# Kernel tuning notes

Hardware: AMD Instinct MI355X
Metric: run time of the kernel (lower is better)

Reference implementation:

```python
import jax, jax.numpy as jnp
import numpy as np

B, N, C = 16, 1024, 768
D = 512
DEPTH = 4
K = 3
HP = WP = 32
A_EPS = 1e-4
POW_MIN = 1e-20
LN_EPS = 1e-5


def setup_inputs() -> dict:
    key = jax.random.key(0)
    ks = jax.random.split(key, 20)
    inp = {
        "tokens": jax.random.normal(ks[0], (B, N, C), dtype=jnp.float32),
        "in_proj_w": jax.random.normal(ks[1], (C, D), dtype=jnp.float32) * 0.02,
        "in_proj_b": jnp.zeros((D,), dtype=jnp.float32),
        "blk_norm_w": jnp.ones((DEPTH, D), dtype=jnp.float32),
        "blk_norm_b": jnp.zeros((DEPTH, D), dtype=jnp.float32),
        "blk_inp_w": jax.random.normal(ks[2], (DEPTH, D, 2 * D), dtype=jnp.float32) * 0.02,
        "blk_inp_b": jnp.zeros((DEPTH, 2 * D), dtype=jnp.float32),
        "blk_conv_w": jax.random.normal(ks[3], (DEPTH, K, K, 1, D), dtype=jnp.float32) * 0.1,
        "blk_conv_b": jnp.zeros((DEPTH, D), dtype=jnp.float32),
        "blk_a_logit": jax.random.normal(ks[4], (DEPTH, D), dtype=jnp.float32) * 0.1,
        "blk_b": jnp.ones((DEPTH, D), dtype=jnp.float32) + jax.random.normal(ks[5], (DEPTH, D), dtype=jnp.float32) * 0.02,
        "blk_c": jnp.ones((DEPTH, D), dtype=jnp.float32) + jax.random.normal(ks[6], (DEPTH, D), dtype=jnp.float32) * 0.02,
        "blk_d": jnp.ones((DEPTH, D), dtype=jnp.float32) + jax.random.normal(ks[7], (DEPTH, D), dtype=jnp.float32) * 0.02,
        "blk_out_w": jax.random.normal(ks[8], (DEPTH, D, D), dtype=jnp.float32) * 0.02,
        "blk_out_b": jnp.zeros((DEPTH, D), dtype=jnp.float32),
        "out_norm_w": jnp.ones((D,), dtype=jnp.float32),
        "out_norm_b": jnp.zeros((D,), dtype=jnp.float32),
    }
    return inp


def _layernorm(x, w, b):
    mu = jnp.mean(x, axis=-1, keepdims=True)
    var = jnp.var(x, axis=-1, keepdims=True)
    return (x - mu) * jax.lax.rsqrt(var + LN_EPS) * w + b


def _ssm_scan(x, a_logit, bb, cc, dd):
    # x: (B', L, D)   s_t = a s_{t-1} + b x_t ; y_t = c s_t + d x_t  (log-domain cumsum form)
    L = x.shape[1]
    a = jnp.clip(jax.nn.sigmoid(a_logit), A_EPS, 1.0 - A_EPS)
    t = jnp.arange(L, dtype=jnp.float32)
    a_pow = jnp.maximum(jnp.exp(t[:, None] * jnp.log(a)[None, :]), POW_MIN)  # (L, D)
    u = x * bb  # (B', L, D)
    r = jnp.cumsum(u / a_pow[None], axis=1)
    s = r * a_pow[None]
    return s * cc + x * dd


def _scan2d(x, a_logit, bb, cc, dd):
    # x: (B, H, W, D); bidirectional row-major + col-major scans, averaged
    Bb, H, W, Dd = x.shape
    L = H * W
    seq_row = x.reshape(Bb, L, Dd)
    seq_col = jnp.transpose(x, (0, 2, 1, 3)).reshape(Bb, L, Dd)
    seqs = jnp.concatenate([seq_row, seq_col], axis=0)            # (2B, L, D)
    all_seqs = jnp.concatenate([seqs, seqs[:, ::-1]], axis=0)     # (4B, L, D)
    y2 = _ssm_scan(all_seqs, a_logit, bb, cc, dd)
    y_f, y_rev = jnp.split(y2, 2, axis=0)
    y = 0.5 * (y_f + y_rev[:, ::-1])
    y_row, y_col = jnp.split(y, 2, axis=0)
    y_row_map = y_row.reshape(Bb, H, W, Dd)
    y_col_map = jnp.transpose(y_col.reshape(Bb, W, H, Dd), (0, 2, 1, 3))
    return 0.5 * (y_row_map + y_col_map)


def _dwconv_silu(x, kernel, bias):
    # x: (B,H,W,D); kernel: (K,K,1,D) depthwise; SAME padding (odd k)
    y = jax.lax.conv_general_dilated(
        x, kernel, window_strides=(1, 1), padding="SAME",
        feature_group_count=x.shape[-1],
        dimension_numbers=("NHWC", "HWIO", "NHWC"))
    return jax.nn.silu(y + bias)


def _block(x, nw, nb, iw, ib, cw, cb, al, sb, sc, sd, ow, ob):
    h = _layernorm(x, nw, nb)
    xg = h @ iw + ib                      # (B,H,W,2D)
    x_in, gate = jnp.split(xg, 2, axis=-1)
    gate = jax.nn.sigmoid(gate)
    u = _dwconv_silu(x_in, cw, cb)
    y = _scan2d(u, al, sb, sc, sd)
    y = (y * gate) @ ow + ob
    return x + y


def reference(tokens, in_proj_w, in_proj_b, blk_norm_w, blk_norm_b, blk_inp_w,
              blk_inp_b, blk_conv_w, blk_conv_b, blk_a_logit, blk_b, blk_c,
              blk_d, blk_out_w, blk_out_b, out_norm_w, out_norm_b):
    x = tokens @ in_proj_w + in_proj_b          # (B, N, D)
    x = x.reshape(B, HP, WP, D)                 # token grid
    for i in range(DEPTH):
        x = _block(x, blk_norm_w[i], blk_norm_b[i], blk_inp_w[i], blk_inp_b[i],
                   blk_conv_w[i], blk_conv_b[i], blk_a_logit[i], blk_b[i],
                   blk_c[i], blk_d[i], blk_out_w[i], blk_out_b[i])
    x = _layernorm(x, out_norm_w, out_norm_b)
    return jnp.mean(x, axis=(1, 2))             # pooled global vector (B, D)
```

## Files before the change

kernel.cpp:

```cpp
#include <hip/hip_runtime.h>
#include <hip/hip_bf16.h>
#include <math.h>

#define NPOS 16384
#define DD   512
#define PP   ((size_t)NPOS * DD)

typedef __bf16 bf16x8 __attribute__((ext_vector_type(8)));
typedef float  f32x4  __attribute__((ext_vector_type(4)));

__device__ __forceinline__ void gload16(const __bf16* g, __bf16* l) {
  __builtin_amdgcn_global_load_lds((__attribute__((address_space(1))) void*)(g),
                                   (__attribute__((address_space(3))) void*)(l), 16, 0, 0);
}
__device__ __forceinline__ void wait_vm0() { asm volatile("s_waitcnt vmcnt(0)" ::: "memory"); }
__device__ __forceinline__ void wait_vm4() { asm volatile("s_waitcnt vmcnt(4)" ::: "memory"); }
__device__ __forceinline__ void wait_lgkm0() { asm volatile("s_waitcnt lgkmcnt(0)" ::: "memory"); }

__global__ __launch_bounds__(256, 3) void gemm_k(
    const __bf16* __restrict__ A, const __bf16* __restrict__ Bt,
    const float* __restrict__ bias, const float* __restrict__ res,
    float* __restrict__ C0, __bf16* __restrict__ C1, __bf16* __restrict__ C1b,
    int N, int K, int epi)
{
  __shared__ __bf16 Asm[3][128 * 32];
  __shared__ __bf16 Bsm[3][128 * 32];

  const int tid  = threadIdx.x;
  const int w    = tid >> 6;
  const int lane = tid & 63;
  const int quad = lane >> 4;
  const int l16  = lane & 15;
  const int wm   = (w >> 1) << 6;
  const int wn   = (w & 1) << 6;

  const int nwg = gridDim.x;
  const int cpx = nwg >> 3;
  const int lin = (blockIdx.x & 7) * cpx + (blockIdx.x >> 3);
  const int nbn = N >> 7;
  const int sh  = (nbn == 8) ? 3 : 2;
  const int mt  = lin >> sh;
  const int ntc = lin & (nbn - 1);
  const int bm  = mt << 7;
  const int bn  = ntc << 7;

  const __bf16* Ab = A  + (size_t)bm * K;
  const __bf16* Bb = Bt + (size_t)bn * K;
  const int nk = K >> 5;

  f32x4 acc[4][4];
  #pragma unroll
  for (int i = 0; i < 4; ++i)
    #pragma unroll
    for (int j = 0; j < 4; ++j) acc[i][j] = (f32x4){0.f, 0.f, 0.f, 0.f};

  #define STG(P, gb, tile, buf, k2) {                                           \
    const int ch_ = tid + ((k2) << 8);                                          \
    const int r_ = ch_ >> 2, c_ = ch_ & 3;                                      \
    gload16(gb + (size_t)r_ * K + ((tile) << 5) + ((c_ ^ ((r_ >> 1) & 3)) << 3),\
            &P[buf][ch_ << 3]);                                                 \
  }

  STG(Asm, Ab, 0, 0, 0) STG(Asm, Ab, 0, 0, 1)
  STG(Bsm, Bb, 0, 0, 0) STG(Bsm, Bb, 0, 0, 1)
  STG(Asm, Ab, 1, 1, 0) STG(Asm, Ab, 1, 1, 1)
  STG(Bsm, Bb, 1, 1, 0) STG(Bsm, Bb, 1, 1, 1)
  wait_vm4();
  __builtin_amdgcn_s_barrier();

  int cur = 0;
  for (int t = 0; t < nk; ++t) {
    const int nx2 = (cur == 0) ? 2 : cur - 1;
    const bool st = (t + 2 < nk);

    if (st) {
      STG(Asm, Ab, t + 2, nx2, 0) STG(Asm, Ab, t + 2, nx2, 1)
      STG(Bsm, Bb, t + 2, nx2, 0) STG(Bsm, Bb, t + 2, nx2, 1)
    }

    bf16x8 af[4], bfr[4];
    #pragma unroll
    for (int i = 0; i < 4; ++i) {
      const int m = wm + i * 16 + l16;
      af[i] = *(const bf16x8*)(&Asm[cur][m * 32 + ((quad ^ ((m >> 1) & 3)) << 3)]);
    }
    #pragma unroll
    for (int j = 0; j < 4; ++j) {
      const int n = wn + j * 16 + l16;
      bfr[j] = *(const bf16x8*)(&Bsm[cur][n * 32 + ((quad ^ ((n >> 1) & 3)) << 3)]);
    }

    __builtin_amdgcn_s_setprio(1);
    #pragma unroll
    for (int i = 0; i < 4; ++i)
      #pragma unroll
      for (int j = 0; j < 4; ++j)
        acc[i][j] = __builtin_amdgcn_mfma_f32_16x16x32_bf16(af[i], bfr[j], acc[i][j], 0, 0, 0);
    __builtin_amdgcn_s_setprio(0);

    if (st) { wait_vm4(); } else { wait_vm0(); }
    __builtin_amdgcn_s_barrier();
    cur = (cur == 2) ? 0 : cur + 1;
  }
  #undef STG

  if (epi == 1) {
    const bool dosig = (bn >= 512);
    __bf16* dst = dosig ? C1 : C1b;
    const int cb = dosig ? (bn - 512) : bn;
    char* wb = (char*)Asm + w * 9216;
    #pragma unroll
    for (int i = 0; i < 4; ++i)
      #pragma unroll
      for (int j = 0; j < 4; ++j) {
        const float bv = bias[bn + wn + j * 16 + l16];
        #pragma unroll
        for (int r = 0; r < 4; ++r) {
          float v = acc[i][j][r] + bv;
          if (dosig) v = 1.f / (1.f + expf(-v));
          *(__bf16*)(wb + (i * 16 + quad * 4 + r) * 144 + (j * 16 + l16) * 2) = (__bf16)v;
        }
      }
    wait_lgkm0();
    #pragma unroll
    for (int i = 0; i < 4; ++i)
      #pragma unroll
      for (int h = 0; h < 2; ++h) {
        const int rr = (lane >> 3) + h * 8;
        bf16x8 vv = *(bf16x8*)(wb + (i * 16 + rr) * 144 + (lane & 7) * 16);
        const int grow = bm + wm + i * 16 + rr;
        *(bf16x8*)(dst + (size_t)grow * 512 + cb + wn + (lane & 7) * 8) = vv;
      }
  } else {
    #pragma unroll
    for (int j = 0; j < 4; ++j) {
      const int col = wn + j * 16 + l16;
      const float bv = bias[bn + col];
      #pragma unroll
      for (int i = 0; i < 4; ++i) {
        const int row0 = bm + wm + i * 16 + quad * 4;
        #pragma unroll
        for (int r = 0; r < 4; ++r) {
          float v = acc[i][j][r] + bv;
          size_t off = (size_t)(row0 + r) * N + bn + col;
          if (epi == 2) v += res[off];
          C0[off] = v;
        }
      }
    }
  }
}

__global__ __launch_bounds__(256) void cvt_k(const float* __restrict__ s, __bf16* __restrict__ d)
{
  size_t i = ((size_t)blockIdx.x * 256 + threadIdx.x) * 8;
  float4 a = *(const float4*)(s + i);
  float4 b = *(const float4*)(s + i + 4);
  bf16x8 v;
  v[0] = (__bf16)a.x; v[1] = (__bf16)a.y; v[2] = (__bf16)a.z; v[3] = (__bf16)a.w;
  v[4] = (__bf16)b.x; v[5] = (__bf16)b.y; v[6] = (__bf16)b.z; v[7] = (__bf16)b.w;
  *(bf16x8*)(d + i) = v;
}

__global__ __launch_bounds__(256) void tr_k(const float* __restrict__ src, __bf16* __restrict__ dst,
                                            int K, int N, size_t sstr, size_t dstr)
{
  __shared__ float t[32][33];
  const float* s = src + blockIdx.z * sstr;
  __bf16* d = dst + blockIdx.z * dstr;
  int n0 = blockIdx.x * 32, k0 = blockIdx.y * 32;
  int tx = threadIdx.x & 31, ty = threadIdx.x >> 5;
  #pragma unroll
  for (int i = 0; i < 4; ++i)
    t[ty + i * 8][tx] = s[(size_t)(k0 + ty + i * 8) * N + n0 + tx];
  __syncthreads();
  #pragma unroll
  for (int i = 0; i < 4; ++i)
    d[(size_t)(n0 + ty + i * 8) * K + k0 + tx] = (__bf16)t[tx][ty + i * 8];
}

__global__ __launch_bounds__(256) void ln_k(const float* __restrict__ x, const float* __restrict__ w,
                                            const float* __restrict__ bv, __bf16* __restrict__ out)
{
  int gw = (blockIdx.x * 256 + threadIdx.x) >> 6;
  int lane = threadIdx.x & 63;
  const float* xp = x + ((size_t)gw << 9) + lane * 8;
  float4 u0 = *(const float4*)xp;
  float4 u1 = *(const float4*)(xp + 4);
  float v[8] = {u0.x,u0.y,u0.z,u0.w,u1.x,u1.y,u1.z,u1.w};
  float s = 0.f;
  #pragma unroll
  for (int j = 0; j < 8; ++j) s += v[j];
  #pragma unroll
  for (int off = 32; off; off >>= 1) s += __shfl_xor(s, off, 64);
  float mu = s * (1.f/512.f);
  float q = 0.f;
  #pragma unroll
  for (int j = 0; j < 8; ++j) { float d = v[j] - mu; q += d*d; }
  #pragma unroll
  for (int off = 32; off; off >>= 1) q += __shfl_xor(q, off, 64);
  float rstd = rsqrtf(q * (1.f/512.f) + 1e-5f);
  int dch = lane * 8;
  float4 w0 = *(const float4*)(w + dch),  w1 = *(const float4*)(w + dch + 4);
  float4 b0 = *(const float4*)(bv + dch), b1 = *(const float4*)(bv + dch + 4);
  float wv[8] = {w0.x,w0.y,w0.z,w0.w,w1.x,w1.y,w1.z,w1.w};
  float bb[8] = {b0.x,b0.y,b0.z,b0.w,b1.x,b1.y,b1.z,b1.w};
  bf16x8 ov;
  #pragma unroll
  for (int j = 0; j < 8; ++j) ov[j] = (__bf16)((v[j] - mu) * rstd * wv[j] + bb[j]);
  *(bf16x8*)(out + ((size_t)gw << 9) + dch) = ov;
}

__device__ __forceinline__ float sig_a(float al) {
  float a = 1.f / (1.f + expf(-al));
  return fminf(fmaxf(a, 1e-4f), 1.f - 1e-4f);
}

__global__ __launch_bounds__(512, 2) void scan2d_k(
    const __bf16* __restrict__ xin, const float* __restrict__ cw, const float* __restrict__ cb,
    const float* __restrict__ alog, const float* __restrict__ bvec, const float* __restrict__ cvec,
    const float* __restrict__ dvec, const __bf16* __restrict__ gate, __bf16* __restrict__ yo)
{
  __shared__ __bf16 T[32768];
  __shared__ __bf16 Y[32768];
  __shared__ float  S[4][32][32];
  const int tid = threadIdx.x;
  const int cg  = blockIdx.x;
  const int b   = blockIdx.y;
  const int ch  = tid & 31;
  const int c0  = tid >> 5;
  const int c1  = c0 + 16;
  const int d   = (cg << 5) + ch;

  const float a   = sig_a(alog[d]);
  const float lna = logf(a);
  const float ia  = 1.f / a;
  const float bb  = bvec[d];
  const float sc  = 0.25f * cvec[d];
  const float dd  = dvec[d];

  const __bf16* ub = xin + ((size_t)b << 19) + (cg << 5);

  #pragma unroll
  for (int i = 0; i < 8; ++i) {
    int flat = (tid + i * 512) << 3;
    int pos = flat >> 5;
    int c8  = flat & 31;
    *(bf16x8*)(T + flat) = *(const bf16x8*)(ub + (size_t)pos * 512 + c8);
  }
  float w00 = cw[(0 << 9) + d], w01 = cw[(1 << 9) + d], w02 = cw[(2 << 9) + d];
  float w10 = cw[(3 << 9) + d], w11 = cw[(4 << 9) + d], w12 = cw[(5 << 9) + d];
  float w20 = cw[(6 << 9) + d], w21 = cw[(7 << 9) + d], w22 = cw[(8 << 9) + d];
  const float cbv = cb[d];
  const float A0f = expf((float)(c0 << 5) * lna),        R0f = expf((float)(c0 << 5) * -lna);
  const float A1f = expf((float)(c1 << 5) * lna),        R1f = expf((float)(c1 << 5) * -lna);
  const float A0b = expf((float)((31 - c0) << 5) * lna), R0b = expf((float)((31 - c0) << 5) * -lna);
  const float A1b = expf((float)((31 - c1) << 5) * lna), R1b = expf((float)((31 - c1) << 5) * -lna);
  __syncthreads();

  {
    const bool up0 = (c0 > 0);
    const bool dn1 = (c0 < 15);
    float a0 = 0.f, a1 = 0.f, a2 = 0.f, f0 = 0.f, f1 = 0.f, f2 = 0.f;
    float b0 = up0 ? (float)T[(((c0 - 1) << 5)) * 32 + ch] : 0.f;
    float b1 =        (float)T[((c0 << 5)) * 32 + ch];
    float b2 =        (float)T[(((c0 + 1) << 5)) * 32 + ch];
    float g0 =        (float)T[(((c1 - 1) << 5)) * 32 + ch];
    float g1 =        (float)T[((c1 << 5)) * 32 + ch];
    float g2 = dn1 ? (float)T[(((c1 + 1) << 5)) * 32 + ch] : 0.f;
    #pragma unroll 4
    for (int ww = 0; ww < 32; ++ww) {
      float e0 = 0.f, e1 = 0.f, e2 = 0.f, i0 = 0.f, i1 = 0.f, i2 = 0.f;
      if (ww < 31) {
        e0 = up0 ? (float)T[(((c0 - 1) << 5) + ww + 1) * 32 + ch] : 0.f;
        e1 =        (float)T[((c0 << 5) + ww + 1) * 32 + ch];
        e2 =        (float)T[(((c0 + 1) << 5) + ww + 1) * 32 + ch];
        i0 =        (float)T[(((c1 - 1) << 5) + ww + 1) * 32 + ch];
        i1 =        (float)T[((c1 << 5) + ww + 1) * 32 + ch];
        i2 = dn1 ? (float)T[(((c1 + 1) << 5) + ww + 1) * 32 + ch] : 0.f;
      }
      float acc0 = cbv, acc1 = cbv;
      acc0 = fmaf(a0, w00, acc0); acc0 = fmaf(b0, w01, acc0); acc0 = fmaf(e0, w02, acc0);
      acc0 = fmaf(a1, w10, acc0); acc0 = fmaf(b1, w11, acc0); acc0 = fmaf(e1, w12, acc0);
      acc0 = fmaf(a2, w20, acc0); acc0 = fmaf(b2, w21, acc0); acc0 = fmaf(e2, w22, acc0);
      acc1 = fmaf(f0, w00, acc1); acc1 = fmaf(g0, w01, acc1); acc1 = fmaf(i0, w02, acc1);
      acc1 = fmaf(f1, w10, acc1); acc1 = fmaf(g1, w11, acc1); acc1 = fmaf(i1, w12, acc1);
      acc1 = fmaf(f2, w20, acc1); acc1 = fmaf(g2, w21, acc1); acc1 = fmaf(i2, w22, acc1);
      acc0 = acc0 / (1.f + expf(-acc0));
      acc1 = acc1 / (1.f + expf(-acc1));
      Y[((c0 << 5) + ww) * 32 + ch] = (__bf16)acc0;
      Y[((c1 << 5) + ww) * 32 + ch] = (__bf16)acc1;
      a0 = b0; a1 = b1; a2 = b2; b0 = e0; b1 = e1; b2 = e2;
      f0 = g0; f1 = g1; f2 = g2; g0 = i0; g1 = i1; g2 = i2;
    }
  }
  __syncthreads();

  #define STEP(r_, uu_, apr_, rp_)                                 \
    { float rr_ = (apr_ < 1e-20f) ? 1e20f : rp_;                   \
      r_ = fmaf((uu_) * bb, rr_, r_); }

  {
    float p0 = A0f, q0 = R0f, p0B = A0b, q0B = R0b;
    float p1 = A1f, q1 = R1f, p1B = A1b, q1B = R1b;
    float s0 = 0.f, s1 = 0.f, s2 = 0.f, s3 = 0.f;
    float s4 = 0.f, s5 = 0.f, s6 = 0.f, s7 = 0.f;
    #pragma unroll 4
    for (int j = 0; j < 32; ++j) {
      float u0rf = (float)Y[((c0 << 5) + j) * 32 + ch];
      float u0rb = (float)Y[((c0 << 5) + (31 - j)) * 32 + ch];
      float u0cf = (float)Y[((j << 5) | c0) * 32 + ch];
      float u0cb = (float)Y[(((31 - j) << 5) | c0) * 32 + ch];
      float u1rf = (float)Y[((c1 << 5) + j) * 32 + ch];
      float u1rb = (float)Y[((c1 << 5) + (31 - j)) * 32 + ch];
      float u1cf = (float)Y[((j << 5) | c1) * 32 + ch];
      float u1cb = (float)Y[(((31 - j) << 5) | c1) * 32 + ch];
      STEP(s0, u0rf, p0, q0)  STEP(s2, u0cf, p0, q0)
      STEP(s1, u0rb, p0B, q0B) STEP(s3, u0cb, p0B, q0B)
      STEP(s4, u1rf, p1, q1)  STEP(s6, u1cf, p1, q1)
      STEP(s5, u1rb, p1B, q1B) STEP(s7, u1cb, p1B, q1B)
      p0 *= a; q0 *= ia; p0B *= a; q0B *= ia;
      p1 *= a; q1 *= ia; p1B *= a; q1B *= ia;
    }
    S[0][c0][ch] = s0; S[1][c0][ch] = s1; S[2][c0][ch] = s2; S[3][c0][ch] = s3;
    S[0][c1][ch] = s4; S[1][c1][ch] = s5; S[2][c1][ch] = s6; S[3][c1][ch] = s7;
  }
  __syncthreads();

  if (tid < 128) {
    int arr = tid >> 5, ch2 = tid & 31;
    float run = 0.f;
    if ((arr & 1) == 0) {
      #pragma unroll 4
      for (int cc = 0; cc < 32; ++cc) { float v = S[arr][cc][ch2]; S[arr][cc][ch2] = run; run += v; }
    } else {
      #pragma unroll 4
      for (int cc = 31; cc >= 0; --cc) { float v = S[arr][cc][ch2]; S[arr][cc][ch2] = run; run += v; }
    }
  }
  __syncthreads();

  {
    float r0 = S[2][c0][ch], r1 = S[2][c1][ch];
    float p0 = A0f, q0 = R0f, p1 = A1f, q1 = R1f;
    #pragma unroll 4
    for (int j = 0; j < 32; ++j) {
      int i0 = ((j << 5) | c0) * 32 + ch, i1 = ((j << 5) | c1) * 32 + ch;
      float u0 = (float)Y[i0], u1 = (float)Y[i1];
      float ap0 = fmaxf(p0, 1e-20f), ap1 = fmaxf(p1, 1e-20f);
      STEP(r0, u0, p0, q0) STEP(r1, u1, p1, q1)
      T[i0] = (__bf16)(r0 * ap0);
      T[i1] = (__bf16)(r1 * ap1);
      p0 *= a; q0 *= ia; p1 *= a; q1 *= ia;
    }
  }
  {
    float r0 = S[3][c0][ch], r1 = S[3][c1][ch];
    float p0 = A0b, q0 = R0b, p1 = A1b, q1 = R1b;
    #pragma unroll 4
    for (int j = 31; j >= 0; --j) {
      int i0 = ((j << 5) | c0) * 32 + ch, i1 = ((j << 5) | c1) * 32 + ch;
      float u0 = (float)Y[i0], u1 = (float)Y[i1];
      float ap0 = fmaxf(p0, 1e-20f), ap1 = fmaxf(p1, 1e-20f);
      STEP(r0, u0, p0, q0) STEP(r1, u1, p1, q1)
      T[i0] = (__bf16)(sc * ((float)T[i0] + r0 * ap0));
      T[i1] = (__bf16)(sc * ((float)T[i1] + r1 * ap1));
      p0 *= a; q0 *= ia; p1 *= a; q1 *= ia;
    }
  }
  __syncthreads();

  {
    float r0 = S[0][c0][ch], r1 = S[0][c1][ch];
    float p0 = A0f, q0 = R0f, p1 = A1f, q1 = R1f;
    #pragma unroll 4
    for (int j = 0; j < 32; ++j) {
      int i0 = ((c0 << 5) + j) * 32 + ch, i1 = ((c1 << 5) + j) * 32 + ch;
      float u0 = (float)Y[i0], u1 = (float)Y[i1];
      float ap0 = fmaxf(p0, 1e-20f), ap1 = fmaxf(p1, 1e-20f);
      STEP(r0, u0, p0, q0) STEP(r1, u1, p1, q1)
      T[i0] = (__bf16)((float)T[i0] + sc * (r0 * ap0));
      T[i1] = (__bf16)((float)T[i1] + sc * (r1 * ap1));
      p0 *= a; q0 *= ia; p1 *= a; q1 *= ia;
    }
  }
  {
    const __bf16* gb = gate + ((size_t)b << 19) + (cg << 5) + ch;
    __bf16* yb = yo + ((size_t)b << 19) + (cg << 5) + ch;
    float r0 = S[1][c0][ch], r1 = S[1][c1][ch];
    float p0 = A0b, q0 = R0b, p1 = A1b, q1 = R1b;
    #pragma unroll 4
    for (int j = 31; j >= 0; --j) {
      int pp0 = (c0 << 5) + j, pp1 = (c1 << 5) + j;
      int i0 = pp0 * 32 + ch, i1 = pp1 * 32 + ch;
      float u0 = (float)Y[i0], u1 = (float)Y[i1];
      float ap0 = fmaxf(p0, 1e-20f), ap1 = fmaxf(p1, 1e-20f);
      STEP(r0, u0, p0, q0) STEP(r1, u1, p1, q1)
      float y0 = (float)T[i0] + sc * (r0 * ap0) + dd * u0;
      float y1 = (float)T[i1] + sc * (r1 * ap1) + dd * u1;
      yb[(size_t)pp0 * 512] = (__bf16)(y0 * (float)gb[(size_t)pp0 * 512]);
      yb[(size_t)pp1 * 512] = (__bf16)(y1 * (float)gb[(size_t)pp1 * 512]);
      p0 *= a; q0 *= ia; p1 *= a; q1 *= ia;
    }
  }
  #undef STEP
}

__global__ __launch_bounds__(256) void reduce_k(const __bf16* __restrict__ hn, float* __restrict__ out)
{
  __shared__ float part[4][64];
  int l = threadIdx.x & 63;
  int q = threadIdx.x >> 6;
  int d = blockIdx.y * 64 + l;
  int b = blockIdx.x;
  const __bf16* p = hn + ((size_t)b << 19) + d + ((size_t)(q * 256) << 9);
  float s0 = 0.f, s1 = 0.f, s2 = 0.f, s3 = 0.f;
  for (int t = 0; t < 256; t += 4) {
    s0 += (float)p[(size_t)(t+0) << 9];
    s1 += (float)p[(size_t)(t+1) << 9];
    s2 += (float)p[(size_t)(t+2) << 9];
    s3 += (float)p[(size_t)(t+3) << 9];
  }
  part[q][l] = (s0 + s1) + (s2 + s3);
  __syncthreads();
  if (threadIdx.x < 64)
    out[b * 512 + d] = (part[0][l] + part[1][l] + part[2][l] + part[3][l]) * (1.f / 1024.f);
}

extern "C" void kernel_launch(void* const* d_in, const int* in_sizes, int n_in,
                              void* d_out, int out_size, void* d_ws, size_t ws_size,
                              hipStream_t stream)
{
  const float* tokens = (const float*)d_in[0];
  const float* in_w   = (const float*)d_in[1];
  const float* in_b   = (const float*)d_in[2];
  const float* nw     = (const float*)d_in[3];
  const float* nb     = (const float*)d_in[4];
  const float* iw     = (const float*)d_in[5];
  const float* ib     = (const float*)d_in[6];
  const float* cw     = (const float*)d_in[7];
  const float* cb     = (const float*)d_in[8];
  const float* al     = (const float*)d_in[9];
  const float* bbv    = (const float*)d_in[10];
  const float* ccv    = (const float*)d_in[11];
  const float* ddv    = (const float*)d_in[12];
  const float* ow     = (const float*)d_in[13];
  const float* obv    = (const float*)d_in[14];
  const float* onw    = (const float*)d_in[15];
  const float* onb    = (const float*)d_in[16];

  float*  x     = (float*)d_ws;
  __bf16* hy16  = (__bf16*)(x + PP);
  __bf16* xin16 = hy16 + PP;
  __bf16* g16   = xin16 + PP;
  __bf16* iwT   = g16 + PP;
  __bf16* owT   = iwT + (size_t)4 * 1024 * 512;
  __bf16* tb16  = owT + (size_t)4 * 512 * 512;
  __bf16* inwT  = xin16;

  cvt_k<<<6144, 256, 0, stream>>>(tokens, tb16);
  tr_k<<<dim3(16, 24, 1), 256, 0, stream>>>(in_w, inwT, 768, 512, 0, 0);
  tr_k<<<dim3(32, 16, 4), 256, 0, stream>>>(iw, iwT, 512, 1024, (size_t)512*1024, (size_t)1024*512);
  tr_k<<<dim3(16, 16, 4), 256, 0, stream>>>(ow, owT, 512, 512, (size_t)512*512, (size_t)512*512);

  gemm_k<<<512, 256, 0, stream>>>(tb16, inwT, in_b, nullptr, x, nullptr, nullptr,
                                  512, 768, 0);

  for (int i = 0; i < 4; ++i) {
    ln_k<<<4096, 256, 0, stream>>>(x, nw + i*512, nb + i*512, hy16);
    gemm_k<<<1024, 256, 0, stream>>>(hy16, iwT + (size_t)i*1024*512, ib + i*1024,
                                     nullptr, nullptr, g16, xin16, 1024, 512, 1);
    scan2d_k<<<dim3(16, 16), 512, 0, stream>>>(xin16, cw + i*9*512, cb + i*512,
                                               al + i*512, bbv + i*512, ccv + i*512,
                                               ddv + i*512, g16, hy16);
    gemm_k<<<512, 256, 0, stream>>>(hy16, owT + (size_t)i*512*512, obv + i*512,
                                    x, x, nullptr, nullptr, 512, 512, 2);
  }

  ln_k<<<4096, 256, 0, stream>>>(x, onw, onb, hy16);
  reduce_k<<<dim3(16, 8), 256, 0, stream>>>(hy16, (float*)d_out);
}
```

Before: 641.1 us.

## Split scan2d into 16-channel blocks with padded LDS rows and more occupancy

The 2D scan kernel now processes 16 channels per block instead of 32, launching twice as many blocks (32x16). Each thread owns one grid row/column instead of two, which halves per-thread work and register pressure, and launch bounds move to 4 blocks per CU. Shared-memory tiles are stored with a padded row stride (544) to reduce bank conflicts, and block-to-channel-group mapping is permuted. The trade-offs are less per-thread ILP, narrower 16-byte global loads per position, and smaller per-block coalescing width for the gated output writes.

```diff
diff --git a/kernel.cpp b/kernel.cpp
--- a/kernel.cpp
+++ b/kernel.cpp
@@ -216,21 +216,23 @@
   return fminf(fmaxf(a, 1e-4f), 1.f - 1e-4f);
 }
 
-__global__ __launch_bounds__(512, 2) void scan2d_k(
+#define CST 544
+
+__global__ __launch_bounds__(512, 4) void scan2d_k(
     const __bf16* __restrict__ xin, const float* __restrict__ cw, const float* __restrict__ cb,
     const float* __restrict__ alog, const float* __restrict__ bvec, const float* __restrict__ cvec,
     const float* __restrict__ dvec, const __bf16* __restrict__ gate, __bf16* __restrict__ yo)
 {
-  __shared__ __bf16 T[32768];
-  __shared__ __bf16 Y[32768];
-  __shared__ float  S[4][32][32];
+  __shared__ __bf16 T[32 * CST];
+  __shared__ __bf16 Y[32 * CST];
+  __shared__ float  S[4][32][16];
   const int tid = threadIdx.x;
-  const int cg  = blockIdx.x;
+  const int bx  = blockIdx.x;
+  const int cg  = ((bx & 7) << 2) | (bx >> 3);
   const int b   = blockIdx.y;
-  const int ch  = tid & 31;
-  const int c0  = tid >> 5;
-  const int c1  = c0 + 16;
-  const int d   = (cg << 5) + ch;
+  const int ch  = tid & 15;
+  const int c0  = tid >> 4;
+  const int d   = (cg << 4) + ch;
 
   const float a   = sig_a(alog[d]);
   const float lna = logf(a);
@@ -239,59 +241,45 @@
   const float sc  = 0.25f * cvec[d];
   const float dd  = dvec[d];
 
-  const __bf16* ub = xin + ((size_t)b << 19) + (cg << 5);
-
-  #pragma unroll
-  for (int i = 0; i < 8; ++i) {
-    int flat = (tid + i * 512) << 3;
-    int pos = flat >> 5;
-    int c8  = flat & 31;
-    *(bf16x8*)(T + flat) = *(const bf16x8*)(ub + (size_t)pos * 512 + c8);
+  const __bf16* ub = xin + ((size_t)b << 19) + (cg << 4);
+
+  #pragma unroll
+  for (int i = 0; i < 4; ++i) {
+    int f = tid + i * 512;
+    int pos = f >> 1, half = f & 1;
+    *(bf16x8*)(T + (pos >> 5) * CST + ((pos & 31) << 4) + (half << 3))
+        = *(const bf16x8*)(ub + (size_t)pos * 512 + (half << 3));
   }
   float w00 = cw[(0 << 9) + d], w01 = cw[(1 << 9) + d], w02 = cw[(2 << 9) + d];
   float w10 = cw[(3 << 9) + d], w11 = cw[(4 << 9) + d], w12 = cw[(5 << 9) + d];
   float w20 = cw[(6 << 9) + d], w21 = cw[(7 << 9) + d], w22 = cw[(8 << 9) + d];
   const float cbv = cb[d];
   const float A0f = expf((float)(c0 << 5) * lna),        R0f = expf((float)(c0 << 5) * -lna);
-  const float A1f = expf((float)(c1 << 5) * lna),        R1f = expf((float)(c1 << 5) * -lna);
   const float A0b = expf((float)((31 - c0) << 5) * lna), R0b = expf((float)((31 - c0) << 5) * -lna);
-  const float A1b = expf((float)((31 - c1) << 5) * lna), R1b = expf((float)((31 - c1) << 5) * -lna);
-  __syncthreads();
-
-  {
-    const bool up0 = (c0 > 0);
-    const bool dn1 = (c0 < 15);
-    float a0 = 0.f, a1 = 0.f, a2 = 0.f, f0 = 0.f, f1 = 0.f, f2 = 0.f;
-    float b0 = up0 ? (float)T[(((c0 - 1) << 5)) * 32 + ch] : 0.f;
-    float b1 =        (float)T[((c0 << 5)) * 32 + ch];
-    float b2 =        (float)T[(((c0 + 1) << 5)) * 32 + ch];
-    float g0 =        (float)T[(((c1 - 1) << 5)) * 32 + ch];
-    float g1 =        (float)T[((c1 << 5)) * 32 + ch];
-    float g2 = dn1 ? (float)T[(((c1 + 1) << 5)) * 32 + ch] : 0.f;
+  __syncthreads();
+
+  {
+    const bool up = (c0 > 0);
+    const bool dn = (c0 < 31);
+    float a0 = 0.f, a1 = 0.f, a2 = 0.f;
+    float b0 = up ? (float)T[(c0 - 1) * CST + ch] : 0.f;
+    float b1 =      (float)T[c0 * CST + ch];
+    float b2 = dn ? (float)T[(c0 + 1) * CST + ch] : 0.f;
     #pragma unroll 4
     for (int ww = 0; ww < 32; ++ww) {
-      float e0 = 0.f, e1 = 0.f, e2 = 0.f, i0 = 0.f, i1 = 0.f, i2 = 0.f;
+      float e0 = 0.f, e1 = 0.f, e2 = 0.f;
       if (ww < 31) {
-        e0 = up0 ? (float)T[(((c0 - 1) << 5) + ww + 1) * 32 + ch] : 0.f;
-        e1 =        (float)T[((c0 << 5) + ww + 1) * 32 + ch];
-        e2 =        (float)T[(((c0 + 1) << 5) + ww + 1) * 32 + ch];
-        i0 =        (float)T[(((c1 - 1) << 5) + ww + 1) * 32 + ch];
-        i1 =        (float)T[((c1 << 5) + ww + 1) * 32 + ch];
-        i2 = dn1 ? (float)T[(((c1 + 1) << 5) + ww + 1) * 32 + ch] : 0.f;
+        e0 = up ? (float)T[(c0 - 1) * CST + ((ww + 1) << 4) + ch] : 0.f;
+        e1 =      (float)T[c0 * CST + ((ww + 1) << 4) + ch];
+        e2 = dn ? (float)T[(c0 + 1) * CST + ((ww + 1) << 4) + ch] : 0.f;
       }
-      float acc0 = cbv, acc1 = cbv;
+      float acc0 = cbv;
       acc0 = fmaf(a0, w00, acc0); acc0 = fmaf(b0, w01, acc0); acc0 = fmaf(e0, w02, acc0);
       acc0 = fmaf(a1, w10, acc0); acc0 = fmaf(b1, w11, acc0); acc0 = fmaf(e1, w12, acc0);
       acc0 = fmaf(a2, w20, acc0); acc0 = fmaf(b2, w21, acc0); acc0 = fmaf(e2, w22, acc0);
-      acc1 = fmaf(f0, w00, acc1); acc1 = fmaf(g0, w01, acc1); acc1 = fmaf(i0, w02, acc1);
-      acc1 = fmaf(f1, w10, acc1); acc1 = fmaf(g1, w11, acc1); acc1 = fmaf(i1, w12, acc1);
-      acc1 = fmaf(f2, w20, acc1); acc1 = fmaf(g2, w21, acc1); acc1 = fmaf(i2, w22, acc1);
       acc0 = acc0 / (1.f + expf(-acc0));
-      acc1 = acc1 / (1.f + expf(-acc1));
-      Y[((c0 << 5) + ww) * 32 + ch] = (__bf16)acc0;
-      Y[((c1 << 5) + ww) * 32 + ch] = (__bf16)acc1;
+      Y[c0 * CST + (ww << 4) + ch] = (__bf16)acc0;
       a0 = b0; a1 = b1; a2 = b2; b0 = e0; b1 = e1; b2 = e2;
-      f0 = g0; f1 = g1; f2 = g2; g0 = i0; g1 = i1; g2 = i2;
     }
   }
   __syncthreads();
@@ -301,34 +289,24 @@
       r_ = fmaf((uu_) * bb, rr_, r_); }
 
   {
-    float p0 = A0f, q0 = R0f, p0B = A0b, q0B = R0b;
-    float p1 = A1f, q1 = R1f, p1B = A1b, q1B = R1b;
+    float pf = A0f, qf = R0f, pb = A0b, qb = R0b;
     float s0 = 0.f, s1 = 0.f, s2 = 0.f, s3 = 0.f;
-    float s4 = 0.f, s5 = 0.f, s6 = 0.f, s7 = 0.f;
     #pragma unroll 4
     for (int j = 0; j < 32; ++j) {
-      float u0rf = (float)Y[((c0 << 5) + j) * 32 + ch];
-      float u0rb = (float)Y[((c0 << 5) + (31 - j)) * 32 + ch];
-      float u0cf = (float)Y[((j << 5) | c0) * 32 + ch];
-      float u0cb = (float)Y[(((31 - j) << 5) | c0) * 32 + ch];
-      float u1rf = (float)Y[((c1 << 5) + j) * 32 + ch];
-      float u1rb = (float)Y[((c1 << 5) + (31 - j)) * 32 + ch];
-      float u1cf = (float)Y[((j << 5) | c1) * 32 + ch];
-      float u1cb = (float)Y[(((31 - j) << 5) | c1) * 32 + ch];
-      STEP(s0, u0rf, p0, q0)  STEP(s2, u0cf, p0, q0)
-      STEP(s1, u0rb, p0B, q0B) STEP(s3, u0cb, p0B, q0B)
-      STEP(s4, u1rf, p1, q1)  STEP(s6, u1cf, p1, q1)
-      STEP(s5, u1rb, p1B, q1B) STEP(s7, u1cb, p1B, q1B)
-      p0 *= a; q0 *= ia; p0B *= a; q0B *= ia;
-      p1 *= a; q1 *= ia; p1B *= a; q1B *= ia;
+      float urf = (float)Y[c0 * CST + (j << 4) + ch];
+      float urb = (float)Y[c0 * CST + ((31 - j) << 4) + ch];
+      float ucf = (float)Y[j * CST + (c0 << 4) + ch];
+      float ucb = (float)Y[(31 - j) * CST + (c0 << 4) + ch];
+      STEP(s0, urf, pf, qf)  STEP(s2, ucf, pf, qf)
+      STEP(s1, urb, pb, qb)  STEP(s3, ucb, pb, qb)
+      pf *= a; qf *= ia; pb *= a; qb *= ia;
     }
     S[0][c0][ch] = s0; S[1][c0][ch] = s1; S[2][c0][ch] = s2; S[3][c0][ch] = s3;
-    S[0][c1][ch] = s4; S[1][c1][ch] = s5; S[2][c1][ch] = s6; S[3][c1][ch] = s7;
-  }
-  __syncthreads();
-
-  if (tid < 128) {
-    int arr = tid >> 5, ch2 = tid & 31;
+  }
+  __syncthreads();
+
+  if (tid < 64) {
+    int arr = tid >> 4, ch2 = tid & 15;
     float run = 0.f;
     if ((arr & 1) == 0) {
       #pragma unroll 4
@@ -341,66 +319,61 @@
   __syncthreads();
 
   {
-    float r0 = S[2][c0][ch], r1 = S[2][c1][ch];
-    float p0 = A0f, q0 = R0f, p1 = A1f, q1 = R1f;
+    float r = S[2][c0][ch];
+    float p = A0f, q = R0f;
     #pragma unroll 4
     for (int j = 0; j < 32; ++j) {
-      int i0 = ((j << 5) | c0) * 32 + ch, i1 = ((j << 5) | c1) * 32 + ch;
-      float u0 = (float)Y[i0], u1 = (float)Y[i1];
-      float ap0 = fmaxf(p0, 1e-20f), ap1 = fmaxf(p1, 1e-20f);
-      STEP(r0, u0, p0, q0) STEP(r1, u1, p1, q1)
-      T[i0] = (__bf16)(r0 * ap0);
-      T[i1] = (__bf16)(r1 * ap1);
-      p0 *= a; q0 *= ia; p1 *= a; q1 *= ia;
-    }
-  }
-  {
-    float r0 = S[3][c0][ch], r1 = S[3][c1][ch];
-    float p0 = A0b, q0 = R0b, p1 = A1b, q1 = R1b;
+      int i0 = j * CST + (c0 << 4) + ch;
+      float u = (float)Y[i0];
+      float ap = fmaxf(p, 1e-20f);
+      STEP(r, u, p, q)
+      T[i0] = (__bf16)(r * ap);
+      p *= a; q *= ia;
+    }
+  }
+  {
+    float r = S[3][c0][ch];
+    float p = A0b, q = R0b;
     #pragma unroll 4
     for (int j = 31; j >= 0; --j) {
-      int i0 = ((j << 5) | c0) * 32 + ch, i1 = ((j << 5) | c1) * 32 + ch;
-      float u0 = (float)Y[i0], u1 = (float)Y[i1];
-      float ap0 = fmaxf(p0, 1e-20f), ap1 = fmaxf(p1, 1e-20f);
-      STEP(r0, u0, p0, q0) STEP(r1, u1, p1, q1)
-      T[i0] = (__bf16)(sc * ((float)T[i0] + r0 * ap0));
-      T[i1] = (__bf16)(sc * ((float)T[i1] + r1 * ap1));
-      p0 *= a; q0 *= ia; p1 *= a; q1 *= ia;
-    }
-  }
-  __syncthreads();
-
-  {
-    float r0 = S[0][c0][ch], r1 = S[0][c1][ch];
-    float p0 = A0f, q0 = R0f, p1 = A1f, q1 = R1f;
+      int i0 = j * CST + (c0 << 4) + ch;
+      float u = (float)Y[i0];
+      float ap = fmaxf(p, 1e-20f);
+      STEP(r, u, p, q)
+      T[i0] = (__bf16)(sc * ((float)T[i0] + r * ap));
+      p *= a; q *= ia;
+    }
+  }
+  __syncthreads();
+
+  {
+    float r = S[0][c0][ch];
+    float p = A0f, q = R0f;
     #pragma unroll 4
     for (int j = 0; j < 32; ++j) {
-      int i0 = ((c0 << 5) + j) * 32 + ch, i1 = ((c1 << 5) + j) * 32 + ch;
-      float u0 = (float)Y[i0], u1 = (float)Y[i1];
-      float ap0 = fmaxf(p0, 1e-20f), ap1 = fmaxf(p1, 1e-20f);
-      STEP(r0, u0, p0, q0) STEP(r1, u1, p1, q1)
-      T[i0] = (__bf16)((float)T[i0] + sc * (r0 * ap0));
-      T[i1] = (__bf16)((float)T[i1] + sc * (r1 * ap1));
-      p0 *= a; q0 *= ia; p1 *= a; q1 *= ia;
-    }
-  }
-  {
-    const __bf16* gb = gate + ((size_t)b << 19) + (cg << 5) + ch;
-    __bf16* yb = yo + ((size_t)b << 19) + (cg << 5) + ch;
-    float r0 = S[1][c0][ch], r1 = S[1][c1][ch];
-    float p0 = A0b, q0 = R0b, p1 = A1b, q1 = R1b;
+      int i0 = c0 * CST + (j << 4) + ch;
+      float u = (float)Y[i0];
+      float ap = fmaxf(p, 1e-20f);
+      STEP(r, u, p, q)
+      T[i0] = (__bf16)((float)T[i0] + sc * (r * ap));
+      p *= a; q *= ia;
+    }
+  }
+  {
+    const __bf16* gb = gate + ((size_t)b << 19) + (cg << 4) + ch;
+    __bf16* yb = yo + ((size_t)b << 19) + (cg << 4) + ch;
+    float r = S[1][c0][ch];
+    float p = A0b, q = R0b;
     #pragma unroll 4
     for (int j = 31; j >= 0; --j) {
-      int pp0 = (c0 << 5) + j, pp1 = (c1 << 5) + j;
-      int i0 = pp0 * 32 + ch, i1 = pp1 * 32 + ch;
-      float u0 = (float)Y[i0], u1 = (float)Y[i1];
-      float ap0 = fmaxf(p0, 1e-20f), ap1 = fmaxf(p1, 1e-20f);
-      STEP(r0, u0, p0, q0) STEP(r1, u1, p1, q1)
-      float y0 = (float)T[i0] + sc * (r0 * ap0) + dd * u0;
-      float y1 = (float)T[i1] + sc * (r1 * ap1) + dd * u1;
-      yb[(size_t)pp0 * 512] = (__bf16)(y0 * (float)gb[(size_t)pp0 * 512]);
-      yb[(size_t)pp1 * 512] = (__bf16)(y1 * (float)gb[(size_t)pp1 * 512]);
-      p0 *= a; q0 *= ia; p1 *= a; q1 *= ia;
+      int pp = (c0 << 5) + j;
+      int i0 = c0 * CST + (j << 4) + ch;
+      float u = (float)Y[i0];
+      float ap = fmaxf(p, 1e-20f);
+      STEP(r, u, p, q)
+      float y0 = (float)T[i0] + sc * (r * ap) + dd * u;
+      yb[(size_t)pp * 512] = (__bf16)(y0 * (float)gb[(size_t)pp * 512]);
+      p *= a; q *= ia;
     }
   }
   #undef STEP
@@ -470,7 +443,7 @@
     ln_k<<<4096, 256, 0, stream>>>(x, nw + i*512, nb + i*512, hy16);
     gemm_k<<<1024, 256, 0, stream>>>(hy16, iwT + (size_t)i*1024*512, ib + i*1024,
                                      nullptr, nullptr, g16, xin16, 1024, 512, 1);
-    scan2d_k<<<dim3(16, 16), 512, 0, stream>>>(xin16, cw + i*9*512, cb + i*512,
+    scan2d_k<<<dim3(32, 16), 512, 0, stream>>>(xin16, cw + i*9*512, cb + i*512,
                                                al + i*512, bbv + i*512, ccv + i*512,
                                                ddv + i*512, g16, hy16);
     gemm_k<<<512, 256, 0, stream>>>(hy16, owT + (size_t)i*512*512, obv + i*512,
```

Result: faster. 605.0 us (-5.6%).
